# Kernel optimization log

Hardware: AMD Instinct MI355X
Metric: run time of the kernel (lower is better)

## Reference

```python
import jax, jax.numpy as jnp
import numpy as np

# Config constants (from init_kwargs)
RADIUS_UPDATE_RATE = 0.01
MIN_RADIUS = 0.1
MAX_RADIUS = 2.0
EPS = 1e-6


def _finite(x, fallback):
    """nan/inf guard: replace non-finite entries with fallback (same math as torch.where(isnan|isinf,...))."""
    bad = jnp.isnan(x) | jnp.isinf(x)
    return jnp.where(bad, fallback, x)


def _compute_score(r, causal=True):
    """QuantumAttention.compute_score: relu'd 2-D dot-product interaction,
    causal mask, row-normalized. r: [B,S,2] -> score: [B,S,S]."""
    raw = jnp.einsum('bse,bte->bst', r, r)          # thin bmm, inner dim 2
    score = jax.nn.relu(raw)
    if causal:
        S = r.shape[1]
        mask = jnp.tril(jnp.ones((S, S), dtype=bool))
        score = jnp.where(mask[None, :, :], score, 0.0)
    denom = jnp.clip(jnp.sum(score, axis=-1, keepdims=True), EPS, None)
    return score / denom


def setup_inputs() -> dict:
    key = jax.random.key(0)
    k1, k2 = jax.random.split(key)
    B, S = 4, 4096
    r_embed = jax.random.normal(k1, (B, S, 2), dtype=jnp.float32)
    # dt in a realistic (dt_scale .. dt_max) range
    dt = jax.random.uniform(k2, (B,), dtype=jnp.float32, minval=1e-4, maxval=1e-2)
    return {"r_embed": r_embed, "dt": dt}


def reference(r_embed, dt):
    # Heun-Euler integration step with radius rescale.
    dt_e = dt[:, None, None]                         # [B,1,1]

    # Stage 1 (k1)
    score = _compute_score(r_embed, causal=True)     # [B,S,S]
    context = jnp.einsum('bst,bte->bse', score, r_embed)
    k1 = _finite(dt_e * context, 0.0)
    r_mid = _finite(r_embed + k1, r_embed)

    # Stage 2 (k2)
    score_mid = _compute_score(r_mid, causal=True)
    context_mid = jnp.einsum('bst,bte->bse', score_mid, r_mid)
    k2 = _finite(dt_e * context_mid, 0.0)

    # Final update + radius adjustment
    r_new = r_embed + 0.5 * (k1 + k2)
    new_radius = jnp.clip(jnp.linalg.norm(r_new, axis=-1, keepdims=True), EPS, None)
    radius_adjustment = jnp.sum(score, axis=-1, keepdims=True) * RADIUS_UPDATE_RATE
    adjusted_radius = jnp.clip(new_radius + radius_adjustment, MIN_RADIUS, MAX_RADIUS)
    scale_factor = adjusted_radius / new_radius
    r_final = r_new * scale_factor
    r_final = _finite(r_final, r_embed)
    return r_final, score
```

## Files before the change

kernel.cpp:

```cpp
#include <hip/hip_runtime.h>
#include <math.h>


#define S_LEN 4096
#define ROWS  16384
#define BLK   256
#define EPSF  1e-6f
#define RATE  0.01f
#define MINR  0.1f
#define MAXR  2.0f

__device__ __forceinline__ void reduce3(float &a, float &b, float &c, float* red) {
    #pragma unroll
    for (int off = 32; off > 0; off >>= 1) {
        a += __shfl_down(a, off);
        b += __shfl_down(b, off);
        c += __shfl_down(c, off);
    }
    const int wave = threadIdx.x >> 6;
    if ((threadIdx.x & 63) == 0) { red[wave*3] = a; red[wave*3+1] = b; red[wave*3+2] = c; }
    __syncthreads();
    if (threadIdx.x == 0) {
        a = red[0] + red[3] + red[6] + red[9];
        b = red[1] + red[4] + red[7] + red[10];
        c = red[2] + red[5] + red[8] + red[11];
    }
}


__global__ __launch_bounds__(BLK) void k_pass1(
    const float2* __restrict__ r_in,
    const float* __restrict__ dt_in,
    float* __restrict__ ws,
    float* __restrict__ score_out)
{
    __shared__ float red[12];
    __shared__ float bc[1];

    const int row = blockIdx.x;
    const int b = row >> 12;
    const int s = row & (S_LEN - 1);
    const float2* rb = r_in + ((size_t)b << 12);
    const float4* rb4 = (const float4*)rb;
    const float2 rs = rb[s];

    float dsum = 0.f, nx = 0.f, ny = 0.f;
    for (int i = threadIdx.x; 2*i <= s; i += BLK) {
        float4 p = rb4[i];
        float d0 = fmaxf(rs.x * p.x + rs.y * p.y, 0.f);
        dsum += d0; nx = fmaf(d0, p.x, nx); ny = fmaf(d0, p.y, ny);
        if (2*i + 1 <= s) {
            float d1 = fmaxf(rs.x * p.z + rs.y * p.w, 0.f);
            dsum += d1; nx = fmaf(d1, p.z, nx); ny = fmaf(d1, p.w, ny);
        }
    }
    reduce3(dsum, nx, ny, red);
    if (threadIdx.x == 0) {
        const float D  = dsum;
        const float dc = fmaxf(D, EPSF);
        const float dtb = dt_in[b];
        float k1x = dtb * nx / dc;
        float k1y = dtb * ny / dc;
        if (!isfinite(k1x)) k1x = 0.f;
        if (!isfinite(k1y)) k1y = 0.f;
        float rmx = rs.x + k1x, rmy = rs.y + k1y;
        if (!isfinite(rmx)) rmx = rs.x;
        if (!isfinite(rmy)) rmy = rs.y;
        float* rmid = ws;
        float* k1w  = ws + 2 * ROWS;
        float* s1w  = ws + 4 * ROWS;
        rmid[2*row]   = rmx; rmid[2*row+1] = rmy;
        k1w[2*row]    = k1x; k1w[2*row+1]  = k1y;
        s1w[row]      = D / dc;
        bc[0]         = 1.f / dc;
    }
    __syncthreads();
    const float inv = bc[0];
    const float isx = rs.x * inv, isy = rs.y * inv;

    float* orow = score_out + (size_t)row * S_LEN;
    #pragma unroll
    for (int q = 0; q < 4; q++) {
        const int t0 = (threadIdx.x << 2) + (q << 10);
        float4 v = make_float4(0.f, 0.f, 0.f, 0.f);
        if (t0 <= s) {
            float4 p01 = rb4[t0 >> 1];
            float4 p23 = rb4[(t0 >> 1) + 1];
            v.x = fmaxf(isx * p01.x + isy * p01.y, 0.f);
            v.y = (t0 + 1 <= s) ? fmaxf(isx * p01.z + isy * p01.w, 0.f) : 0.f;
            v.z = (t0 + 2 <= s) ? fmaxf(isx * p23.x + isy * p23.y, 0.f) : 0.f;
            v.w = (t0 + 3 <= s) ? fmaxf(isx * p23.z + isy * p23.w, 0.f) : 0.f;
        }
        *((float4*)(orow + t0)) = v;
    }
}

__global__ __launch_bounds__(BLK) void k_pass2(
    const float2* __restrict__ r_in,
    const float* __restrict__ dt_in,
    const float* __restrict__ ws,
    float* __restrict__ rfinal_out)
{
    __shared__ float red[12];

    const int row = blockIdx.x;
    const int b = row >> 12;
    const int s = row & (S_LEN - 1);
    const float2* rm = ((const float2*)ws) + ((size_t)b << 12);
    const float4* rm4 = (const float4*)rm;
    const float2 rs = rm[s];

    float dsum = 0.f, nx = 0.f, ny = 0.f;
    for (int i = threadIdx.x; 2*i <= s; i += BLK) {
        float4 p = rm4[i];
        float d0 = fmaxf(rs.x * p.x + rs.y * p.y, 0.f);
        dsum += d0; nx = fmaf(d0, p.x, nx); ny = fmaf(d0, p.y, ny);
        if (2*i + 1 <= s) {
            float d1 = fmaxf(rs.x * p.z + rs.y * p.w, 0.f);
            dsum += d1; nx = fmaf(d1, p.z, nx); ny = fmaf(d1, p.w, ny);
        }
    }
    reduce3(dsum, nx, ny, red);
    if (threadIdx.x == 0) {
        const float* k1w = ws + 2 * ROWS;
        const float* s1w = ws + 4 * ROWS;
        const float dc = fmaxf(dsum, EPSF);
        const float dtb = dt_in[b];
        float k2x = dtb * nx / dc;
        float k2y = dtb * ny / dc;
        if (!isfinite(k2x)) k2x = 0.f;
        if (!isfinite(k2y)) k2y = 0.f;
        const float2 r0 = r_in[row];
        const float k1x = k1w[2*row], k1y = k1w[2*row+1];
        const float rnx = r0.x + 0.5f * (k1x + k2x);
        const float rny = r0.y + 0.5f * (k1y + k2y);
        const float nr = fmaxf(sqrtf(rnx*rnx + rny*rny), EPSF);
        const float ar = fminf(fmaxf(nr + s1w[row] * RATE, MINR), MAXR);
        const float sc = ar / nr;
        float fx = rnx * sc, fy = rny * sc;
        if (!isfinite(fx)) fx = r0.x;
        if (!isfinite(fy)) fy = r0.y;
        rfinal_out[2*row]   = fx;
        rfinal_out[2*row+1] = fy;
    }
}

extern "C" void kernel_launch(void* const* d_in, const int* in_sizes, int n_in,
                              void* d_out, int out_size, void* d_ws, size_t ws_size,
                              hipStream_t stream) {
    const float2* r_in  = (const float2*)d_in[0];
    const float*  dt_in = (const float*)d_in[1];
    float* out = (float*)d_out;
    float* ws  = (float*)d_ws;

    float* rfinal_out = out;
    float* score_out  = out + (size_t)2 * ROWS;

    hipLaunchKernelGGL(k_pass1, dim3(ROWS), dim3(BLK), 0, stream,
                       r_in, dt_in, ws, score_out);
    hipLaunchKernelGGL(k_pass2, dim3(ROWS), dim3(BLK), 0, stream,
                       r_in, dt_in, ws, rfinal_out);
}
```

Baseline: 273.9 us.

## Map one row per wavefront and use nontemporal stores for score output

Each 64-lane wavefront now handles a whole row instead of one 256-thread block per row. This lets the reduction run entirely with shuffles, with no shared memory or __syncthreads. The score write loop is restructured for 64 lanes, skips loads for fully masked chunks, and uses nontemporal vector stores to avoid polluting cache with the 268MB output. The trade-off is less parallelism per row in the reduction loop, which makes long rows slower per wave and the work balance across waves uneven.

```diff
diff --git a/kernel.cpp b/kernel.cpp
--- a/kernel.cpp
+++ b/kernel.cpp
@@ -10,42 +10,25 @@
 #define MINR  0.1f
 #define MAXR  2.0f
 
-__device__ __forceinline__ void reduce3(float &a, float &b, float &c, float* red) {
-    #pragma unroll
-    for (int off = 32; off > 0; off >>= 1) {
-        a += __shfl_down(a, off);
-        b += __shfl_down(b, off);
-        c += __shfl_down(c, off);
-    }
-    const int wave = threadIdx.x >> 6;
-    if ((threadIdx.x & 63) == 0) { red[wave*3] = a; red[wave*3+1] = b; red[wave*3+2] = c; }
-    __syncthreads();
-    if (threadIdx.x == 0) {
-        a = red[0] + red[3] + red[6] + red[9];
-        b = red[1] + red[4] + red[7] + red[10];
-        c = red[2] + red[5] + red[8] + red[11];
-    }
-}
+typedef float f32x4 __attribute__((ext_vector_type(4)));
 
 
 __global__ __launch_bounds__(BLK) void k_pass1(
     const float2* __restrict__ r_in,
-    const float* __restrict__ dt_in,
+    const float*  __restrict__ dt_in,
     float* __restrict__ ws,
     float* __restrict__ score_out)
 {
-    __shared__ float red[12];
-    __shared__ float bc[1];
-
-    const int row = blockIdx.x;
+    const int lane = threadIdx.x & 63;
+    const int row  = (blockIdx.x << 2) + (threadIdx.x >> 6);
     const int b = row >> 12;
     const int s = row & (S_LEN - 1);
-    const float2* rb = r_in + ((size_t)b << 12);
+    const float2* rb  = r_in + ((size_t)b << 12);
     const float4* rb4 = (const float4*)rb;
     const float2 rs = rb[s];
 
     float dsum = 0.f, nx = 0.f, ny = 0.f;
-    for (int i = threadIdx.x; 2*i <= s; i += BLK) {
+    for (int i = lane; 2*i <= s; i += 64) {
         float4 p = rb4[i];
         float d0 = fmaxf(rs.x * p.x + rs.y * p.y, 0.f);
         dsum += d0; nx = fmaf(d0, p.x, nx); ny = fmaf(d0, p.y, ny);
@@ -54,10 +37,17 @@
             dsum += d1; nx = fmaf(d1, p.z, nx); ny = fmaf(d1, p.w, ny);
         }
     }
-    reduce3(dsum, nx, ny, red);
-    if (threadIdx.x == 0) {
-        const float D  = dsum;
-        const float dc = fmaxf(D, EPSF);
+    #pragma unroll
+    for (int off = 32; off > 0; off >>= 1) {
+        dsum += __shfl_down(dsum, off);
+        nx   += __shfl_down(nx, off);
+        ny   += __shfl_down(ny, off);
+    }
+    const float D   = __shfl(dsum, 0);
+    const float dc  = fmaxf(D, EPSF);
+    const float inv = 1.f / dc;
+
+    if (lane == 0) {
         const float dtb = dt_in[b];
         float k1x = dtb * nx / dc;
         float k1y = dtb * ny / dc;
@@ -66,52 +56,47 @@
         float rmx = rs.x + k1x, rmy = rs.y + k1y;
         if (!isfinite(rmx)) rmx = rs.x;
         if (!isfinite(rmy)) rmy = rs.y;
-        float* rmid = ws;
-        float* k1w  = ws + 2 * ROWS;
-        float* s1w  = ws + 4 * ROWS;
-        rmid[2*row]   = rmx; rmid[2*row+1] = rmy;
-        k1w[2*row]    = k1x; k1w[2*row+1]  = k1y;
-        s1w[row]      = D / dc;
-        bc[0]         = 1.f / dc;
+        ws[2*row]              = rmx;  ws[2*row + 1]              = rmy;
+        ws[2*ROWS + 2*row]     = k1x;  ws[2*ROWS + 2*row + 1]     = k1y;
+        ws[4*ROWS + row]       = D / dc;
     }
-    __syncthreads();
-    const float inv = bc[0];
+
     const float isx = rs.x * inv, isy = rs.y * inv;
-
     float* orow = score_out + (size_t)row * S_LEN;
-    #pragma unroll
-    for (int q = 0; q < 4; q++) {
-        const int t0 = (threadIdx.x << 2) + (q << 10);
-        float4 v = make_float4(0.f, 0.f, 0.f, 0.f);
-        if (t0 <= s) {
-            float4 p01 = rb4[t0 >> 1];
-            float4 p23 = rb4[(t0 >> 1) + 1];
-            v.x = fmaxf(isx * p01.x + isy * p01.y, 0.f);
-            v.y = (t0 + 1 <= s) ? fmaxf(isx * p01.z + isy * p01.w, 0.f) : 0.f;
-            v.z = (t0 + 2 <= s) ? fmaxf(isx * p23.x + isy * p23.y, 0.f) : 0.f;
-            v.w = (t0 + 3 <= s) ? fmaxf(isx * p23.z + isy * p23.w, 0.f) : 0.f;
+    #pragma unroll 4
+    for (int q = 0; q < 16; q++) {
+        const int t0 = (lane << 2) + (q << 8);
+        f32x4 v = (f32x4)(0.f);
+        if ((q << 8) <= s) {
+            if (t0 <= s) {
+                const float4 p01 = rb4[t0 >> 1];
+                const float4 p23 = rb4[(t0 >> 1) + 1];
+                v.x = fmaxf(isx * p01.x + isy * p01.y, 0.f);
+                v.y = (t0 + 1 <= s) ? fmaxf(isx * p01.z + isy * p01.w, 0.f) : 0.f;
+                v.z = (t0 + 2 <= s) ? fmaxf(isx * p23.x + isy * p23.y, 0.f) : 0.f;
+                v.w = (t0 + 3 <= s) ? fmaxf(isx * p23.z + isy * p23.w, 0.f) : 0.f;
+            }
         }
-        *((float4*)(orow + t0)) = v;
+        __builtin_nontemporal_store(v, (f32x4*)(orow + t0));
     }
 }
 
 __global__ __launch_bounds__(BLK) void k_pass2(
     const float2* __restrict__ r_in,
-    const float* __restrict__ dt_in,
-    const float* __restrict__ ws,
+    const float*  __restrict__ dt_in,
+    const float*  __restrict__ ws,
     float* __restrict__ rfinal_out)
 {
-    __shared__ float red[12];
-
-    const int row = blockIdx.x;
+    const int lane = threadIdx.x & 63;
+    const int row  = (blockIdx.x << 2) + (threadIdx.x >> 6);
     const int b = row >> 12;
     const int s = row & (S_LEN - 1);
-    const float2* rm = ((const float2*)ws) + ((size_t)b << 12);
+    const float2* rm  = ((const float2*)ws) + ((size_t)b << 12);
     const float4* rm4 = (const float4*)rm;
     const float2 rs = rm[s];
 
     float dsum = 0.f, nx = 0.f, ny = 0.f;
-    for (int i = threadIdx.x; 2*i <= s; i += BLK) {
+    for (int i = lane; 2*i <= s; i += 64) {
         float4 p = rm4[i];
         float d0 = fmaxf(rs.x * p.x + rs.y * p.y, 0.f);
         dsum += d0; nx = fmaf(d0, p.x, nx); ny = fmaf(d0, p.y, ny);
@@ -120,28 +105,32 @@
             dsum += d1; nx = fmaf(d1, p.z, nx); ny = fmaf(d1, p.w, ny);
         }
     }
-    reduce3(dsum, nx, ny, red);
-    if (threadIdx.x == 0) {
-        const float* k1w = ws + 2 * ROWS;
-        const float* s1w = ws + 4 * ROWS;
-        const float dc = fmaxf(dsum, EPSF);
+    #pragma unroll
+    for (int off = 32; off > 0; off >>= 1) {
+        dsum += __shfl_down(dsum, off);
+        nx   += __shfl_down(nx, off);
+        ny   += __shfl_down(ny, off);
+    }
+
+    if (lane == 0) {
+        const float dc  = fmaxf(dsum, EPSF);
         const float dtb = dt_in[b];
         float k2x = dtb * nx / dc;
         float k2y = dtb * ny / dc;
         if (!isfinite(k2x)) k2x = 0.f;
         if (!isfinite(k2y)) k2y = 0.f;
-        const float2 r0 = r_in[row];
-        const float k1x = k1w[2*row], k1y = k1w[2*row+1];
+        const float2 r0  = r_in[row];
+        const float  k1x = ws[2*ROWS + 2*row], k1y = ws[2*ROWS + 2*row + 1];
         const float rnx = r0.x + 0.5f * (k1x + k2x);
         const float rny = r0.y + 0.5f * (k1y + k2y);
-        const float nr = fmaxf(sqrtf(rnx*rnx + rny*rny), EPSF);
-        const float ar = fminf(fmaxf(nr + s1w[row] * RATE, MINR), MAXR);
-        const float sc = ar / nr;
+        const float nr  = fmaxf(sqrtf(rnx*rnx + rny*rny), EPSF);
+        const float ar  = fminf(fmaxf(nr + ws[4*ROWS + row] * RATE, MINR), MAXR);
+        const float sc  = ar / nr;
         float fx = rnx * sc, fy = rny * sc;
         if (!isfinite(fx)) fx = r0.x;
         if (!isfinite(fy)) fy = r0.y;
-        rfinal_out[2*row]   = fx;
-        rfinal_out[2*row+1] = fy;
+        rfinal_out[2*row]     = fx;
+        rfinal_out[2*row + 1] = fy;
     }
 }
 
@@ -156,8 +145,8 @@
     float* rfinal_out = out;
     float* score_out  = out + (size_t)2 * ROWS;
 
-    hipLaunchKernelGGL(k_pass1, dim3(ROWS), dim3(BLK), 0, stream,
+    hipLaunchKernelGGL(k_pass1, dim3(ROWS / 4), dim3(BLK), 0, stream,
                        r_in, dt_in, ws, score_out);
-    hipLaunchKernelGGL(k_pass2, dim3(ROWS), dim3(BLK), 0, stream,
+    hipLaunchKernelGGL(k_pass2, dim3(ROWS / 4), dim3(BLK), 0, stream,
                        r_in, dt_in, ws, rfinal_out);
 }
```

Result: slower. 287.1 us (+4.8%).
